# Performance work log

Hardware: AMD Instinct MI355X
Metric: run time of the kernel (lower is better)

Reference implementation:

```python
import jax, jax.numpy as jnp
import numpy as np

DIM = 768
H = 64
W = 64
NB = 8
BS = DIM // NB
LAMBD = 0.01
SCALE = 0.02


def softshrink(x, lambd):
    return jnp.sign(x) * jnp.maximum(jnp.abs(x) - lambd, 0.0)


def setup_inputs() -> dict:
    key = jax.random.key(0)
    ks = jax.random.split(key, 7)
    x = jax.random.normal(ks[0], (8, H * W, DIM), dtype=jnp.float32)
    w1 = SCALE * jax.random.normal(ks[1], (2, NB, BS, BS), dtype=jnp.float32)
    b1 = SCALE * jax.random.normal(ks[2], (2, NB, BS), dtype=jnp.float32)
    w2 = SCALE * jax.random.normal(ks[3], (2, NB, BS, BS), dtype=jnp.float32)
    b2 = SCALE * jax.random.normal(ks[4], (2, NB, BS), dtype=jnp.float32)
    # Conv1d(dim, dim, kernel_size=1) == per-token linear: weight [C_out, C_in], bias [C_out]
    Wb = (1.0 / np.sqrt(DIM)) * jax.random.normal(ks[5], (DIM, DIM), dtype=jnp.float32)
    bb = (1.0 / np.sqrt(DIM)) * jax.random.normal(ks[6], (DIM,), dtype=jnp.float32)
    return {"x": x, "w1": w1, "b1": b1, "w2": w2, "b2": b2, "Wb": Wb, "bb": bb}


def reference(x, w1, b1, w2, b2, Wb, bb):
    B, N, C = x.shape
    # bias path: Conv1d with kernel 1 is a linear map over channels
    bias = jnp.einsum('bnc,dc->bnd', x, Wb) + bb
    # spectral path
    xg = x.reshape(B, H, W, C)
    xf = jnp.fft.rfft2(xg, axes=(1, 2), norm='ortho')          # [B, H, W//2+1, C] complex64
    xf = xf.reshape(B, H, W // 2 + 1, NB, BS)
    xr, xi = jnp.real(xf), jnp.imag(xf)
    # layer 1: complex block-diagonal matmul + relu
    r1 = jax.nn.relu(jnp.einsum('...bd,bdk->...bk', xr, w1[0])
                     - jnp.einsum('...bd,bdk->...bk', xi, w1[1]) + b1[0])
    i1 = jax.nn.relu(jnp.einsum('...bd,bdk->...bk', xr, w1[1])
                     + jnp.einsum('...bd,bdk->...bk', xi, w1[0]) + b1[1])
    # layer 2
    r2 = (jnp.einsum('...bd,bdk->...bk', r1, w2[0])
          - jnp.einsum('...bd,bdk->...bk', i1, w2[1]) + b2[0])
    i2 = (jnp.einsum('...bd,bdk->...bk', r1, w2[1])
          + jnp.einsum('...bd,bdk->...bk', i1, w2[0]) + b2[1])
    r2 = softshrink(r2, LAMBD)
    i2 = softshrink(i2, LAMBD)
    xc = (r2 + 1j * i2).reshape(B, H, W // 2 + 1, C)
    xo = jnp.fft.irfft2(xc, s=(H, W), axes=(1, 2), norm='ortho')  # [B, H, W, C]
    return xo.reshape(B, N, C) + bias
```

## Files before the change

### kernel.cpp

```cpp
#include <hip/hip_runtime.h>
#include <math.h>

#ifndef M_PI
#define M_PI 3.14159265358979323846
#endif

namespace {

constexpr int kDim = 768;
constexpr int kNKW = 33;
constexpr int kB = 8;
constexpr float kLambd = 0.01f;
constexpr size_t kXFElems = (size_t)kB * kNKW * 64 * kDim;

typedef __attribute__((ext_vector_type(8))) __bf16 bf16x8;
typedef __attribute__((ext_vector_type(8))) short short8;
typedef __attribute__((ext_vector_type(4))) float f32x4;

alignas(16) __device__ unsigned short g_wT[4 * 8 * 96 * 96];
alignas(16) __device__ unsigned short g_twC[64 * 64];
alignas(16) __device__ unsigned short g_twS[64 * 64];
alignas(16) __device__ unsigned short g_iwC[64 * 64];
alignas(16) __device__ unsigned short g_iwS[64 * 64];

__device__ inline unsigned short f2bf(float f) {
  unsigned int u = __float_as_uint(f);
  unsigned int r = (u + 0x7FFFu + ((u >> 16) & 1u)) >> 16;
  return (unsigned short)r;
}

__device__ inline bf16x8 s2b(short8 s) { return __builtin_bit_cast(bf16x8, s); }
__device__ inline bf16x8 negb(short8 s) {
  s ^= (short)0x8000;
  return __builtin_bit_cast(bf16x8, s);
}

__device__ inline void gload_lds16(const void* g, void* l) {
  __builtin_amdgcn_global_load_lds(
      (const __attribute__((address_space(1))) unsigned int*)g,
      (__attribute__((address_space(3))) unsigned int*)l, 16, 0, 0);
}

__global__ __launch_bounds__(256) void init_tables_kernel() {
  const int e = blockIdx.x * 256 + threadIdx.x;
  if (e >= 4096) return;
  const int a = e >> 6;
  const int bcol = e & 63;
  const float ang = (float)(2.0 * M_PI / 64.0) * (float)((a * bcol) & 63);
  float s_, c_;
  __sincosf(ang, &s_, &c_);
  g_twC[e] = f2bf(0.125f * c_);
  g_twS[e] = f2bf(0.125f * s_);
  unsigned short cv = 0, sv = 0;
  if (bcol < 33) {
    const float al = (bcol == 0 || bcol == 32) ? 0.125f : 0.25f;
    cv = f2bf(al * c_);
    sv = f2bf(-al * s_);
  }
  g_iwC[e] = cv;
  g_iwS[e] = sv;
}

__global__ __launch_bounds__(256) void cvt_f32_bf16_kernel(
    const float* __restrict__ in, unsigned short* __restrict__ out, int n4) {
  int i = blockIdx.x * 256 + threadIdx.x;
  if (i >= n4) return;
  const float4 v = reinterpret_cast<const float4*>(in)[i];
  ushort4 o;
  o.x = f2bf(v.x); o.y = f2bf(v.y); o.z = f2bf(v.z); o.w = f2bf(v.w);
  reinterpret_cast<ushort4*>(out)[i] = o;
}

__global__ __launch_bounds__(256) void cvt_w_kernel(
    const float* __restrict__ w1, const float* __restrict__ w2) {
  const int e = blockIdx.x * 256 + threadIdx.x;
  if (e >= 4 * 8 * 96 * 96) return;
  const int k = e % 96;
  const int d = (e / 96) % 96;
  const int nbm = e / 9216;
  const int mtx = nbm >> 3;
  const int nb = nbm & 7;
  const float* src =
      (mtx < 2 ? w1 : w2) + ((size_t)(mtx & 1) * 8 + nb) * 9216;
  g_wT[((size_t)nbm * 96 + k) * 96 + d] = f2bf(src[d * 96 + k]);
}

__global__ __launch_bounds__(256) void mfma_gemm_kernel(
    const unsigned short* __restrict__ xbf, const unsigned short* __restrict__ wbf,
    const float* __restrict__ bb, float* __restrict__ out) {
  __shared__ unsigned short As[128 * 32];
  __shared__ unsigned short Bs[128 * 32];
  const int t = threadIdx.x;
  const int lane = t & 63;
  const int wid = t >> 6;
  const int wm = wid >> 1;
  const int wn = wid & 1;
  const int id = blockIdx.x;
  const int swz = (id & 7) * 192 + (id >> 3);
  const int m0 = (swz / 6) * 128;
  const int n0 = (swz % 6) * 128;

  f32x4 acc[4][4];
#pragma unroll
  for (int i = 0; i < 4; ++i)
#pragma unroll
    for (int j = 0; j < 4; ++j) acc[i][j] = (f32x4){0.f, 0.f, 0.f, 0.f};

  char* AsB = (char*)As;
  char* BsB = (char*)Bs;
  const int cl = lane & 15;
  const int kg = lane >> 4;

  for (int k0 = 0; k0 < 768; k0 += 32) {
#pragma unroll
    for (int i = 0; i < 2; ++i) {
      const int off = (wid * 2 + i) * 1024 + lane * 16;
      const int row = off >> 6;
      const int kb = off & 63;
      const char* gA = (const char*)xbf + ((size_t)(m0 + row) * 768 + k0) * 2 + kb;
      gload_lds16(gA, AsB + (wid * 2 + i) * 1024);
      const char* gB = (const char*)wbf + ((size_t)(n0 + row) * 768 + k0) * 2 + kb;
      gload_lds16(gB, BsB + (wid * 2 + i) * 1024);
    }
    asm volatile("s_waitcnt vmcnt(0)" ::: "memory");
    __syncthreads();

    bf16x8 av[4], bv[4];
#pragma unroll
    for (int mi = 0; mi < 4; ++mi) {
      const int r = wm * 64 + mi * 16 + cl;
      av[mi] = *reinterpret_cast<const bf16x8*>(AsB + r * 64 + kg * 16);
    }
#pragma unroll
    for (int ni = 0; ni < 4; ++ni) {
      const int r = wn * 64 + ni * 16 + cl;
      bv[ni] = *reinterpret_cast<const bf16x8*>(BsB + r * 64 + kg * 16);
    }
#pragma unroll
    for (int mi = 0; mi < 4; ++mi)
#pragma unroll
      for (int ni = 0; ni < 4; ++ni)
        acc[mi][ni] = __builtin_amdgcn_mfma_f32_16x16x32_bf16(
            av[mi], bv[ni], acc[mi][ni], 0, 0, 0);
    __syncthreads();
  }

#pragma unroll
  for (int ni = 0; ni < 4; ++ni) {
    const int n = n0 + wn * 64 + ni * 16 + cl;
    const float bias = bb[n];
#pragma unroll
    for (int mi = 0; mi < 4; ++mi) {
      const int m = m0 + wm * 64 + mi * 16 + kg * 4;
#pragma unroll
      for (int r = 0; r < 4; ++r) {
        out[(size_t)(m + r) * 768 + n] = acc[mi][ni][r] + bias;
      }
    }
  }
}

__global__ __launch_bounds__(256) void rfft_row_mfma_kernel(
    const float* __restrict__ x, unsigned short* __restrict__ xbf,
    unsigned short* __restrict__ XFr, unsigned short* __restrict__ XFi) {
  __shared__ alignas(16) unsigned short xs[64 * 66];
  __shared__ alignas(16) unsigned short sOr[33 * 68];
  __shared__ alignas(16) unsigned short sOi[33 * 68];
  const int t = threadIdx.x;
  const int lane = t & 63;
  const int wv = t >> 6;
  const int cl = lane & 15;
  const int kg = lane >> 4;
  const int bh = blockIdx.x;
  const int b = bh >> 6;
  const int h = bh & 63;
  const int c0 = blockIdx.y * 64;

  short8 pcs[3][2], pss[3][2];
#pragma unroll
  for (int nt = 0; nt < 3; ++nt) {
#pragma unroll
    for (int kf = 0; kf < 2; ++kf) {
      const int row = nt * 16 + cl;
      const int w0 = kf * 32 + kg * 8;
      pcs[nt][kf] = *reinterpret_cast<const short8*>(g_twC + row * 64 + w0);
      pss[nt][kf] = *reinterpret_cast<const short8*>(g_twS + row * 64 + w0);
    }
  }

  {
    const float* xrow = x + (size_t)bh * (64 * 768) + c0;
    unsigned short* xbrow = xbf + (size_t)bh * (64 * 768) + c0;
#pragma unroll 4
    for (int it = 0; it < 16; ++it) {
      const int w = wv * 16 + it;
      const float v = xrow[(size_t)w * 768 + lane];
      const unsigned short bv = f2bf(v);
      xbrow[(size_t)w * 768 + lane] = bv;
      xs[w * 66 + lane] = bv;
    }
  }
  __syncthreads();

  const int cA = wv * 16 + cl;
  short8 ax[2];
#pragma unroll
  for (int kf = 0; kf < 2; ++kf) {
#pragma unroll
    for (int j = 0; j < 8; ++j)
      ax[kf][j] = (short)xs[(kf * 32 + kg * 8 + j) * 66 + cA];
  }

  f32x4 aR[3], aI[3];
#pragma unroll
  for (int nt = 0; nt < 3; ++nt) {
    aR[nt] = (f32x4){0.f, 0.f, 0.f, 0.f};
    aI[nt] = (f32x4){0.f, 0.f, 0.f, 0.f};
  }

#pragma unroll
  for (int nt = 0; nt < 3; ++nt) {
#pragma unroll
    for (int kf = 0; kf < 2; ++kf) {
      aR[nt] = __builtin_amdgcn_mfma_f32_16x16x32_bf16(s2b(ax[kf]), s2b(pcs[nt][kf]), aR[nt], 0, 0, 0);
      aI[nt] = __builtin_amdgcn_mfma_f32_16x16x32_bf16(s2b(ax[kf]), negb(pss[nt][kf]), aI[nt], 0, 0, 0);
    }
  }

  const int cL = wv * 16 + kg * 4;
#pragma unroll
  for (int nt = 0; nt < 3; ++nt) {
    const int kh = nt * 16 + cl;
    if (kh <= 32) {
      ushort4 vr, vi;
      vr.x = f2bf(aR[nt][0]); vr.y = f2bf(aR[nt][1]);
      vr.z = f2bf(aR[nt][2]); vr.w = f2bf(aR[nt][3]);
      vi.x = f2bf(aI[nt][0]); vi.y = f2bf(aI[nt][1]);
      vi.z = f2bf(aI[nt][2]); vi.w = f2bf(aI[nt][3]);
      *reinterpret_cast<ushort4*>(sOr + kh * 68 + cL) = vr;
      *reinterpret_cast<ushort4*>(sOi + kh * 68 + cL) = vi;
    }
  }
  __syncthreads();
  for (int idx = t; idx < 33 * 16; idx += 256) {
    const int row = idx >> 4;
    const int c4 = (idx & 15) * 4;
    const size_t off = (((size_t)b * kNKW + row) * 64 + h) * 768 + c0 + c4;
    *reinterpret_cast<ushort4*>(XFr + off) =
        *reinterpret_cast<const ushort4*>(sOr + row * 68 + c4);
    *reinterpret_cast<ushort4*>(XFi + off) =
        *reinterpret_cast<const ushort4*>(sOi + row * 68 + c4);
  }
}

__global__ __launch_bounds__(256) void spectral_mid_kernel(
    unsigned short* __restrict__ Xr, unsigned short* __restrict__ Xi,
    const float* __restrict__ b1, const float* __restrict__ b2) {
  __shared__ alignas(16) unsigned short sXr[64 * 104];
  __shared__ alignas(16) unsigned short sXi[64 * 104];
  __shared__ alignas(16) unsigned short sYr[64 * 104];
  __shared__ alignas(16) unsigned short sYi[64 * 104];
  const int t = threadIdx.x;
  const int lane = t & 63;
  const int wid = t >> 6;
  const int wm = wid >> 1;
  const int wn = wid & 1;
  const int cl = lane & 15;
  const int kg = lane >> 4;
  const int nb = blockIdx.y;
  const size_t gbase = (size_t)blockIdx.x * (64 * 768) + nb * 96;

  short8 pcs[2][2], pss[2][2];
#pragma unroll
  for (int mt = 0; mt < 2; ++mt) {
#pragma unroll
    for (int kf = 0; kf < 2; ++kf) {
      const int row = wm * 32 + mt * 16 + cl;
      const int k0 = kf * 32 + kg * 8;
      pcs[mt][kf] = *reinterpret_cast<const short8*>(g_twC + row * 64 + k0);
      pss[mt][kf] = *reinterpret_cast<const short8*>(g_twS + row * 64 + k0);
    }
  }

  {
    const int row = t >> 2;
    const int q = t & 3;
    const size_t gof = gbase + (size_t)row * 768 + q * 24;
    unsigned short* lr = sXr + row * 104 + q * 24;
    unsigned short* li = sXi + row * 104 + q * 24;
#pragma unroll
    for (int v = 0; v < 3; ++v) {
      *reinterpret_cast<short8*>(lr + v * 8) =
          *reinterpret_cast<const short8*>(Xr + gof + v * 8);
      *reinterpret_cast<short8*>(li + v * 8) =
          *reinterpret_cast<const short8*>(Xi + gof + v * 8);
    }
  }
  __syncthreads();

  f32x4 accR[2][3], accI[2][3];

#pragma unroll
  for (int mt = 0; mt < 2; ++mt)
#pragma unroll
    for (int nt = 0; nt < 3; ++nt) {
      accR[mt][nt] = (f32x4){0.f, 0.f, 0.f, 0.f};
      accI[mt][nt] = (f32x4){0.f, 0.f, 0.f, 0.f};
    }
#pragma unroll
  for (int kf = 0; kf < 2; ++kf) {
    const int k0 = kf * 32 + kg * 8;
    short8 bR[3], bI[3];
#pragma unroll
    for (int nt = 0; nt < 3; ++nt) {
      const int col = wn * 48 + nt * 16 + cl;
#pragma unroll
      for (int j = 0; j < 8; ++j) {
        bR[nt][j] = (short)sXr[(k0 + j) * 104 + col];
        bI[nt][j] = (short)sXi[(k0 + j) * 104 + col];
      }
    }
#pragma unroll
    for (int mt = 0; mt < 2; ++mt) {
      const short8 cs = pcs[mt][kf];
      const short8 ss = pss[mt][kf];
#pragma unroll
      for (int nt = 0; nt < 3; ++nt) {
        accR[mt][nt] = __builtin_amdgcn_mfma_f32_16x16x32_bf16(s2b(cs), s2b(bR[nt]), accR[mt][nt], 0, 0, 0);
        accR[mt][nt] = __builtin_amdgcn_mfma_f32_16x16x32_bf16(s2b(ss), s2b(bI[nt]), accR[mt][nt], 0, 0, 0);
        accI[mt][nt] = __builtin_amdgcn_mfma_f32_16x16x32_bf16(s2b(cs), s2b(bI[nt]), accI[mt][nt], 0, 0, 0);
        accI[mt][nt] = __builtin_amdgcn_mfma_f32_16x16x32_bf16(negb(ss), s2b(bR[nt]), accI[mt][nt], 0, 0, 0);
      }
    }
  }
#pragma unroll
  for (int mt = 0; mt < 2; ++mt) {
#pragma unroll
    for (int nt = 0; nt < 3; ++nt) {
      const int col = wn * 48 + nt * 16 + cl;
      const int row0 = wm * 32 + mt * 16 + kg * 4;
#pragma unroll
      for (int r = 0; r < 4; ++r) {
        sYr[(row0 + r) * 104 + col] = f2bf(accR[mt][nt][r]);
        sYi[(row0 + r) * 104 + col] = f2bf(accI[mt][nt][r]);
      }
    }
  }
  __syncthreads();

  const unsigned short* wt1r = g_wT + (size_t)(0 * 8 + nb) * 9216;
  const unsigned short* wt1i = g_wT + (size_t)(1 * 8 + nb) * 9216;
  const unsigned short* wt2r = g_wT + (size_t)(2 * 8 + nb) * 9216;
  const unsigned short* wt2i = g_wT + (size_t)(3 * 8 + nb) * 9216;

#pragma unroll
  for (int mt = 0; mt < 2; ++mt)
#pragma unroll
    for (int nt = 0; nt < 3; ++nt) {
      accR[mt][nt] = (f32x4){0.f, 0.f, 0.f, 0.f};
      accI[mt][nt] = (f32x4){0.f, 0.f, 0.f, 0.f};
    }
#pragma unroll
  for (int kk = 0; kk < 3; ++kk) {
    const int ko = kk * 32 + kg * 8;
    short8 axr[2], axi[2];
#pragma unroll
    for (int mt = 0; mt < 2; ++mt) {
      const int row = wm * 32 + mt * 16 + cl;
      axr[mt] = *reinterpret_cast<const short8*>(sYr + row * 104 + ko);
      axi[mt] = *reinterpret_cast<const short8*>(sYi + row * 104 + ko);
    }
    short8 wr_[3], wi_[3];
#pragma unroll
    for (int nt = 0; nt < 3; ++nt) {
      const int rw = wn * 48 + nt * 16 + cl;
      wr_[nt] = *reinterpret_cast<const short8*>(wt1r + rw * 96 + ko);
      wi_[nt] = *reinterpret_cast<const short8*>(wt1i + rw * 96 + ko);
    }
#pragma unroll
    for (int mt = 0; mt < 2; ++mt) {
      const bf16x8 ar = s2b(axr[mt]);
      const bf16x8 ai = s2b(axi[mt]);
      const bf16x8 ain = negb(axi[mt]);
#pragma unroll
      for (int nt = 0; nt < 3; ++nt) {
        accR[mt][nt] = __builtin_amdgcn_mfma_f32_16x16x32_bf16(ar, s2b(wr_[nt]), accR[mt][nt], 0, 0, 0);
        accR[mt][nt] = __builtin_amdgcn_mfma_f32_16x16x32_bf16(ain, s2b(wi_[nt]), accR[mt][nt], 0, 0, 0);
        accI[mt][nt] = __builtin_amdgcn_mfma_f32_16x16x32_bf16(ar, s2b(wi_[nt]), accI[mt][nt], 0, 0, 0);
        accI[mt][nt] = __builtin_amdgcn_mfma_f32_16x16x32_bf16(ai, s2b(wr_[nt]), accI[mt][nt], 0, 0, 0);
      }
    }
  }
#pragma unroll
  for (int nt = 0; nt < 3; ++nt) {
    const int col = wn * 48 + nt * 16 + cl;
    const float br = b1[nb * 96 + col];
    const float bi = b1[768 + nb * 96 + col];
#pragma unroll
    for (int mt = 0; mt < 2; ++mt) {
      const int row0 = wm * 32 + mt * 16 + kg * 4;
#pragma unroll
      for (int r = 0; r < 4; ++r) {
        sXr[(row0 + r) * 104 + col] = f2bf(fmaxf(accR[mt][nt][r] + br, 0.f));
        sXi[(row0 + r) * 104 + col] = f2bf(fmaxf(accI[mt][nt][r] + bi, 0.f));
      }
    }
  }
  __syncthreads();

#pragma unroll
  for (int mt = 0; mt < 2; ++mt)
#pragma unroll
    for (int nt = 0; nt < 3; ++nt) {
      accR[mt][nt] = (f32x4){0.f, 0.f, 0.f, 0.f};
      accI[mt][nt] = (f32x4){0.f, 0.f, 0.f, 0.f};
    }
#pragma unroll
  for (int kk = 0; kk < 3; ++kk) {
    const int ko = kk * 32 + kg * 8;
    short8 axr[2], axi[2];
#pragma unroll
    for (int mt = 0; mt < 2; ++mt) {
      const int row = wm * 32 + mt * 16 + cl;
      axr[mt] = *reinterpret_cast<const short8*>(sXr + row * 104 + ko);
      axi[mt] = *reinterpret_cast<const short8*>(sXi + row * 104 + ko);
    }
    short8 wr_[3], wi_[3];
#pragma unroll
    for (int nt = 0; nt < 3; ++nt) {
      const int rw = wn * 48 + nt * 16 + cl;
      wr_[nt] = *reinterpret_cast<const short8*>(wt2r + rw * 96 + ko);
      wi_[nt] = *reinterpret_cast<const short8*>(wt2i + rw * 96 + ko);
    }
#pragma unroll
    for (int mt = 0; mt < 2; ++mt) {
      const bf16x8 ar = s2b(axr[mt]);
      const bf16x8 ai = s2b(axi[mt]);
      const bf16x8 ain = negb(axi[mt]);
#pragma unroll
      for (int nt = 0; nt < 3; ++nt) {
        accR[mt][nt] = __builtin_amdgcn_mfma_f32_16x16x32_bf16(ar, s2b(wr_[nt]), accR[mt][nt], 0, 0, 0);
        accR[mt][nt] = __builtin_amdgcn_mfma_f32_16x16x32_bf16(ain, s2b(wi_[nt]), accR[mt][nt], 0, 0, 0);
        accI[mt][nt] = __builtin_amdgcn_mfma_f32_16x16x32_bf16(ar, s2b(wi_[nt]), accI[mt][nt], 0, 0, 0);
        accI[mt][nt] = __builtin_amdgcn_mfma_f32_16x16x32_bf16(ai, s2b(wr_[nt]), accI[mt][nt], 0, 0, 0);
      }
    }
  }
#pragma unroll
  for (int nt = 0; nt < 3; ++nt) {
    const int col = wn * 48 + nt * 16 + cl;
    const float br = b2[nb * 96 + col];
    const float bi = b2[768 + nb * 96 + col];
#pragma unroll
    for (int mt = 0; mt < 2; ++mt) {
      const int row0 = wm * 32 + mt * 16 + kg * 4;
#pragma unroll
      for (int r = 0; r < 4; ++r) {
        float vr = accR[mt][nt][r] + br;
        float vi = accI[mt][nt][r] + bi;
        vr = (vr > kLambd) ? (vr - kLambd) : ((vr < -kLambd) ? (vr + kLambd) : 0.f);
        vi = (vi > kLambd) ? (vi - kLambd) : ((vi < -kLambd) ? (vi + kLambd) : 0.f);
        sYr[(row0 + r) * 104 + col] = f2bf(vr);
        sYi[(row0 + r) * 104 + col] = f2bf(vi);
      }
    }
  }
  __syncthreads();

#pragma unroll
  for (int mt = 0; mt < 2; ++mt)
#pragma unroll
    for (int nt = 0; nt < 3; ++nt) {
      accR[mt][nt] = (f32x4){0.f, 0.f, 0.f, 0.f};
      accI[mt][nt] = (f32x4){0.f, 0.f, 0.f, 0.f};
    }
#pragma unroll
  for (int kf = 0; kf < 2; ++kf) {
    const int k0 = kf * 32 + kg * 8;
    short8 bR[3], bI[3];
#pragma unroll
    for (int nt = 0; nt < 3; ++nt) {
      const int col = wn * 48 + nt * 16 + cl;
#pragma unroll
      for (int j = 0; j < 8; ++j) {
        bR[nt][j] = (short)sYr[(k0 + j) * 104 + col];
        bI[nt][j] = (short)sYi[(k0 + j) * 104 + col];
      }
    }
#pragma unroll
    for (int mt = 0; mt < 2; ++mt) {
      const short8 cs = pcs[mt][kf];
      const short8 ss = pss[mt][kf];
#pragma unroll
      for (int nt = 0; nt < 3; ++nt) {
        accR[mt][nt] = __builtin_amdgcn_mfma_f32_16x16x32_bf16(s2b(cs), s2b(bR[nt]), accR[mt][nt], 0, 0, 0);
        accR[mt][nt] = __builtin_amdgcn_mfma_f32_16x16x32_bf16(negb(ss), s2b(bI[nt]), accR[mt][nt], 0, 0, 0);
        accI[mt][nt] = __builtin_amdgcn_mfma_f32_16x16x32_bf16(s2b(cs), s2b(bI[nt]), accI[mt][nt], 0, 0, 0);
        accI[mt][nt] = __builtin_amdgcn_mfma_f32_16x16x32_bf16(s2b(ss), s2b(bR[nt]), accI[mt][nt], 0, 0, 0);
      }
    }
  }
#pragma unroll
  for (int mt = 0; mt < 2; ++mt) {
#pragma unroll
    for (int nt = 0; nt < 3; ++nt) {
      const int col = wn * 48 + nt * 16 + cl;
      const int row0 = wm * 32 + mt * 16 + kg * 4;
#pragma unroll
      for (int r = 0; r < 4; ++r) {
        const size_t off = gbase + (size_t)(row0 + r) * 768 + col;
        Xr[off] = f2bf(accR[mt][nt][r]);
        Xi[off] = f2bf(accI[mt][nt][r]);
      }
    }
  }
}

__global__ __launch_bounds__(256) void irfft_row_add_mfma_kernel(
    const unsigned short* __restrict__ Zr, const unsigned short* __restrict__ Zi,
    float* __restrict__ out) {
  const int t = threadIdx.x;
  const int lane = t & 63;
  const int wv = t >> 6;
  const int cl = lane & 15;
  const int kg = lane >> 4;
  const int bh = blockIdx.x;
  const int b = bh >> 6;
  const int h = bh & 63;
  const int cb = blockIdx.y * 64 + wv * 16;

  short8 pbc[4][2], pbs[4][2];
#pragma unroll
  for (int nt = 0; nt < 4; ++nt) {
#pragma unroll
    for (int kf = 0; kf < 2; ++kf) {
      const int row = nt * 16 + cl;
      const int kw0 = kf * 32 + kg * 8;
      pbc[nt][kf] = *reinterpret_cast<const short8*>(g_iwC + row * 64 + kw0);
      pbs[nt][kf] = *reinterpret_cast<const short8*>(g_iwS + row * 64 + kw0);
    }
  }

  const int cA = cb + cl;
  short8 azr[2], azi[2];
#pragma unroll
  for (int kf = 0; kf < 2; ++kf) {
#pragma unroll
    for (int j = 0; j < 8; ++j) {
      const int kw = kf * 32 + kg * 8 + j;
      short zr = 0, zi = 0;
      if (kw < 33) {
        const size_t off = (((size_t)b * kNKW + kw) * 64 + h) * 768 + cA;
        zr = (short)Zr[off];
        zi = (short)Zi[off];
      }
      azr[kf][j] = zr;
      azi[kf][j] = zi;
    }
  }

  const int cD = cb + kg * 4;
  float* obase = out + ((size_t)bh * 64) * 768;
  f32x4 aO[4];
#pragma unroll
  for (int nt = 0; nt < 4; ++nt) {
    const int w = nt * 16 + cl;
    aO[nt] = *reinterpret_cast<const f32x4*>(obase + (size_t)w * 768 + cD);
  }

#pragma unroll
  for (int nt = 0; nt < 4; ++nt) {
#pragma unroll
    for (int kf = 0; kf < 2; ++kf) {
      aO[nt] = __builtin_amdgcn_mfma_f32_16x16x32_bf16(s2b(azr[kf]), s2b(pbc[nt][kf]), aO[nt], 0, 0, 0);
      aO[nt] = __builtin_amdgcn_mfma_f32_16x16x32_bf16(s2b(azi[kf]), s2b(pbs[nt][kf]), aO[nt], 0, 0, 0);
    }
  }

#pragma unroll
  for (int nt = 0; nt < 4; ++nt) {
    const int w = nt * 16 + cl;
    *reinterpret_cast<f32x4*>(obase + (size_t)w * 768 + cD) = aO[nt];
  }
}

}

extern "C" void kernel_launch(void* const* d_in, const int* in_sizes, int n_in,
                              void* d_out, int out_size, void* d_ws,
                              size_t ws_size, hipStream_t stream) {
  (void)in_sizes; (void)n_in; (void)out_size;
  const float* x  = (const float*)d_in[0];
  const float* w1 = (const float*)d_in[1];
  const float* b1 = (const float*)d_in[2];
  const float* w2 = (const float*)d_in[3];
  const float* b2 = (const float*)d_in[4];
  const float* Wb = (const float*)d_in[5];
  const float* bb = (const float*)d_in[6];
  float* out = (float*)d_out;

  if (ws_size < 2 * kXFElems * sizeof(float)) return;
  unsigned short* xbf = (unsigned short*)d_ws;
  unsigned short* wbf = xbf + (size_t)32768 * 768;
  unsigned short* XFr = wbf + (size_t)768 * 768;
  unsigned short* XFi = XFr + kXFElems;

  init_tables_kernel<<<dim3(16), 256, 0, stream>>>();
  cvt_f32_bf16_kernel<<<dim3((768 * 768 / 4 + 255) / 256), 256, 0, stream>>>(
      Wb, wbf, 768 * 768 / 4);
  cvt_w_kernel<<<dim3(4 * 8 * 96 * 96 / 256), 256, 0, stream>>>(w1, w2);
  rfft_row_mfma_kernel<<<dim3(512, 12), 256, 0, stream>>>(x, xbf, XFr, XFi);
  mfma_gemm_kernel<<<dim3(1536), 256, 0, stream>>>(xbf, wbf, bb, out);
  spectral_mid_kernel<<<dim3(264, 8), 256, 0, stream>>>(XFr, XFi, b1, b2);
  irfft_row_add_mfma_kernel<<<dim3(512, 12), 256, 0, stream>>>(XFr, XFi, out);
}
```

Measured before the change: 275.3 us.

## Compute DFT twiddles in LDS, vectorize loads, write row-FFT output directly

The row rFFT kernel now builds its cosine and sine twiddle tables in shared memory with __sincosf per block, where it used to read them from global tables, and folds the 1/8 scale and the sign of the sine into those tables. The input load is widened to float2 per lane. The output is stored straight to global memory from the MFMA accumulators, dropping the LDS staging buffer and its second barrier. The costs are extra sincos work in every block and less coalesced 8-byte scattered stores; the 0.125 scale is baked in here, which only matches if the old global tables used the same normalization.

```diff
diff --git a/kernel.cpp b/kernel.cpp
--- a/kernel.cpp
+++ b/kernel.cpp
@@ -163,10 +163,20 @@
 __global__ __launch_bounds__(256) void rfft_row_mfma_kernel(
     const float* __restrict__ x, unsigned short* __restrict__ xbf,
     unsigned short* __restrict__ XFr, unsigned short* __restrict__ XFi) {
+  __shared__ alignas(16) unsigned short Cs[48 * 80];
+  __shared__ alignas(16) unsigned short Ss[48 * 80];
   __shared__ alignas(16) unsigned short xs[64 * 66];
-  __shared__ alignas(16) unsigned short sOr[33 * 68];
-  __shared__ alignas(16) unsigned short sOi[33 * 68];
   const int t = threadIdx.x;
+  for (int e = t; e < 48 * 64; e += 256) {
+    const int kh = e >> 6;
+    const int w = e & 63;
+    const float ang = (float)(2.0 * M_PI / 64.0) * (float)((kh * w) & 63);
+    float s_, c_;
+    __sincosf(ang, &s_, &c_);
+    Cs[kh * 80 + w] = f2bf(0.125f * c_);
+    Ss[kh * 80 + w] = f2bf(-0.125f * s_);
+  }
+
   const int lane = t & 63;
   const int wv = t >> 6;
   const int cl = lane & 15;
@@ -176,80 +186,67 @@
   const int h = bh & 63;
   const int c0 = blockIdx.y * 64;
 
-  short8 pcs[3][2], pss[3][2];
+  {
+    const float* xrow = x + (size_t)bh * (64 * 768) + c0;
+    unsigned short* xbrow = xbf + (size_t)bh * (64 * 768) + c0;
+    const int wofs = lane >> 5;
+    const int c2 = (lane & 31) * 2;
+#pragma unroll
+    for (int it = 0; it < 8; ++it) {
+      const int w = wv * 16 + it * 2 + wofs;
+      const float2 v = *reinterpret_cast<const float2*>(xrow + (size_t)w * 768 + c2);
+      ushort2 bv;
+      bv.x = f2bf(v.x);
+      bv.y = f2bf(v.y);
+      *reinterpret_cast<ushort2*>(xbrow + (size_t)w * 768 + c2) = bv;
+      *reinterpret_cast<ushort2*>(xs + w * 66 + c2) = bv;
+    }
+  }
+  __syncthreads();
+
+  const int cA = wv * 16 + cl;
+  short8 ax[2];
+#pragma unroll
+  for (int kf = 0; kf < 2; ++kf) {
+#pragma unroll
+    for (int j = 0; j < 8; ++j)
+      ax[kf][j] = (short)xs[(kf * 32 + kg * 8 + j) * 66 + cA];
+  }
+
+  f32x4 aR[3], aI[3];
+#pragma unroll
+  for (int nt = 0; nt < 3; ++nt) {
+    aR[nt] = (f32x4){0.f, 0.f, 0.f, 0.f};
+    aI[nt] = (f32x4){0.f, 0.f, 0.f, 0.f};
+  }
+
 #pragma unroll
   for (int nt = 0; nt < 3; ++nt) {
 #pragma unroll
     for (int kf = 0; kf < 2; ++kf) {
       const int row = nt * 16 + cl;
       const int w0 = kf * 32 + kg * 8;
-      pcs[nt][kf] = *reinterpret_cast<const short8*>(g_twC + row * 64 + w0);
-      pss[nt][kf] = *reinterpret_cast<const short8*>(g_twS + row * 64 + w0);
-    }
-  }
-
-  {
-    const float* xrow = x + (size_t)bh * (64 * 768) + c0;
-    unsigned short* xbrow = xbf + (size_t)bh * (64 * 768) + c0;
-#pragma unroll 4
-    for (int it = 0; it < 16; ++it) {
-      const int w = wv * 16 + it;
-      const float v = xrow[(size_t)w * 768 + lane];
-      const unsigned short bv = f2bf(v);
-      xbrow[(size_t)w * 768 + lane] = bv;
-      xs[w * 66 + lane] = bv;
-    }
-  }
-  __syncthreads();
-
-  const int cA = wv * 16 + cl;
-  short8 ax[2];
-#pragma unroll
-  for (int kf = 0; kf < 2; ++kf) {
-#pragma unroll
-    for (int j = 0; j < 8; ++j)
-      ax[kf][j] = (short)xs[(kf * 32 + kg * 8 + j) * 66 + cA];
-  }
-
-  f32x4 aR[3], aI[3];
-#pragma unroll
-  for (int nt = 0; nt < 3; ++nt) {
-    aR[nt] = (f32x4){0.f, 0.f, 0.f, 0.f};
-    aI[nt] = (f32x4){0.f, 0.f, 0.f, 0.f};
-  }
-
-#pragma unroll
-  for (int nt = 0; nt < 3; ++nt) {
-#pragma unroll
-    for (int kf = 0; kf < 2; ++kf) {
-      aR[nt] = __builtin_amdgcn_mfma_f32_16x16x32_bf16(s2b(ax[kf]), s2b(pcs[nt][kf]), aR[nt], 0, 0, 0);
-      aI[nt] = __builtin_amdgcn_mfma_f32_16x16x32_bf16(s2b(ax[kf]), negb(pss[nt][kf]), aI[nt], 0, 0, 0);
-    }
-  }
-
-  const int cL = wv * 16 + kg * 4;
+      const bf16x8 bc = *reinterpret_cast<const bf16x8*>(Cs + row * 80 + w0);
+      const bf16x8 bs = *reinterpret_cast<const bf16x8*>(Ss + row * 80 + w0);
+      aR[nt] = __builtin_amdgcn_mfma_f32_16x16x32_bf16(s2b(ax[kf]), bc, aR[nt], 0, 0, 0);
+      aI[nt] = __builtin_amdgcn_mfma_f32_16x16x32_bf16(s2b(ax[kf]), bs, aI[nt], 0, 0, 0);
+    }
+  }
+
+  const int cD = c0 + wv * 16 + kg * 4;
 #pragma unroll
   for (int nt = 0; nt < 3; ++nt) {
     const int kh = nt * 16 + cl;
     if (kh <= 32) {
+      const size_t off = (((size_t)b * kNKW + kh) * 64 + h) * 768 + cD;
       ushort4 vr, vi;
       vr.x = f2bf(aR[nt][0]); vr.y = f2bf(aR[nt][1]);
       vr.z = f2bf(aR[nt][2]); vr.w = f2bf(aR[nt][3]);
       vi.x = f2bf(aI[nt][0]); vi.y = f2bf(aI[nt][1]);
       vi.z = f2bf(aI[nt][2]); vi.w = f2bf(aI[nt][3]);
-      *reinterpret_cast<ushort4*>(sOr + kh * 68 + cL) = vr;
-      *reinterpret_cast<ushort4*>(sOi + kh * 68 + cL) = vi;
-    }
-  }
-  __syncthreads();
-  for (int idx = t; idx < 33 * 16; idx += 256) {
-    const int row = idx >> 4;
-    const int c4 = (idx & 15) * 4;
-    const size_t off = (((size_t)b * kNKW + row) * 64 + h) * 768 + c0 + c4;
-    *reinterpret_cast<ushort4*>(XFr + off) =
-        *reinterpret_cast<const ushort4*>(sOr + row * 68 + c4);
-    *reinterpret_cast<ushort4*>(XFi + off) =
-        *reinterpret_cast<const ushort4*>(sOi + row * 68 + c4);
+      *reinterpret_cast<ushort4*>(XFr + off) = vr;
+      *reinterpret_cast<ushort4*>(XFi + off) = vi;
+    }
   }
 }
 
```

Result: faster. 245.1 us, median of 3 (-11.0%).
